# Optimization experiments

Hardware: AMD Instinct MI355X
Metric: run time of the kernel (lower is better)

Reference implementation:

```python
import jax, jax.numpy as jnp
import numpy as np

H = 1024
IN = 512
B = 32
E_H = 0.5
Z_MIN = 0.001
Z_MAX = 0.1
DT = 1.0


def setup_inputs() -> dict:
    key = jax.random.key(0)
    ks = jax.random.split(key, 10)
    s = 1.0 / np.sqrt(H)
    uni = lambda k, shape: jax.random.uniform(k, shape, jnp.float32, -s, s)
    return {
        "x": jax.random.normal(ks[0], (IN, B), jnp.float32),
        "h": jax.random.uniform(ks[1], (B, H), jnp.float32),      # hidden state [B,H]
        "X": jnp.ones((B, H, H), jnp.float32),                     # resources
        "U": jnp.full((B, H, H), 0.9, jnp.float32),                # utilization (init 0.9)
        "c_x": uni(ks[2], (H, H)),
        "c_u": uni(ks[3], (H, H)),
        "c_U": uni(ks[4], (H, H)),
        "c_h": uni(ks[5], (H, 1)),
        "w": uni(ks[6], (H, H)),
        "p": uni(ks[7], (H, IN)),
        "b": uni(ks[8], (H, 1)),
    }


def reference(x, h, X, U, c_x, c_u, c_U, c_h, w, p, b):
    sig = jax.nn.sigmoid
    hb = h[:, :, None]                                  # h[b,j] broadcast over k -> [B,H,1]
    # resource (X) update: z_x + (1-z_x)*X - dt*U*X*h
    z_x = Z_MIN + (Z_MAX - Z_MIN) * sig(c_x)            # [H,H]
    X_new = z_x + (1.0 - z_x) * X - DT * U * (X * hb)   # [B,H,H]
    # utilization (U) update, clamped to [Ucap (detached), 1]
    z_u = Z_MIN + (Z_MAX - Z_MIN) * sig(c_u)            # [H,H]
    Ucap = 0.9 * sig(c_U)                               # [H,H]
    U_new = Ucap * z_u + (1.0 - z_u) * U + DT * Ucap * ((1.0 - U) * hb)
    U_new = jnp.clip(U_new, jax.lax.stop_gradient(Ucap), 1.0)
    # hidden update with dynamic weights W = w * U * X (per batch)
    z_h = E_H * sig(c_h)                                # [H,1]
    W = w * U_new * X_new                               # [B,H,H]
    rec = jnp.einsum("bjk,bk->jb", W, h)               # [H,B]
    pre = rec + p @ x + b                               # [H,B]
    h_newT = (1.0 - z_h) * h.T + z_h * sig(pre)         # [H,B]
    return h_newT.T                                     # [B,H]
```

## Files before the change

### kernel.cpp

```cpp
#include <hip/hip_runtime.h>

#define HH 1024
#define INW 512
#define BB 32
#define BG 16
#define Z_MIN_C 0.001f
#define Z_RANGE_C 0.099f
#define E_H_C 0.5f

__device__ __forceinline__ float sigmoidf_(float v) {
    return 1.0f / (1.0f + __expf(-v));
}

__global__ __launch_bounds__(256) void stp_fused(
    const float* __restrict__ x,
    const float* __restrict__ h,
    const float* __restrict__ X,
    const float* __restrict__ U,
    const float* __restrict__ c_x,
    const float* __restrict__ c_u,
    const float* __restrict__ c_U,
    const float* __restrict__ c_h,
    const float* __restrict__ w,
    const float* __restrict__ p,
    const float* __restrict__ bias,
    float* __restrict__ out)
{
    const int j = blockIdx.x >> 1;
    const int g = blockIdx.x & 1;
    const int t = threadIdx.x;
    const int lane = t & 63;
    const int wave = t >> 6;

    __shared__ float px_part[16][BG];
    __shared__ float rec_part[BG][4];

    {
        const int b_id = t & 15;
        const int seg = t >> 4;
        float acc = 0.0f;
        const float* prow = p + j * INW + seg * 32;
        const float* xcol = x + seg * 32 * BB + (g * BG + b_id);
        #pragma unroll
        for (int i = 0; i < 32; ++i)
            acc = fmaf(prow[i], xcol[i * BB], acc);
        px_part[seg][b_id] = acc;
    }

    const int k0 = t * 4;
    float4 cx4 = *(const float4*)(c_x + j * HH + k0);
    float4 cu4 = *(const float4*)(c_u + j * HH + k0);
    float4 cC4 = *(const float4*)(c_U + j * HH + k0);
    float4 wv4 = *(const float4*)(w + j * HH + k0);
    const float* cxv = &cx4.x;
    const float* cuv = &cu4.x;
    const float* cCv = &cC4.x;
    const float* wvv = &wv4.x;

    float zx[4], ozx[4], Acoef[4], ozu[4], Uc[4], wr[4];
    #pragma unroll
    for (int c = 0; c < 4; ++c) {
        float zxx = Z_MIN_C + Z_RANGE_C * sigmoidf_(cxv[c]);
        float zuu = Z_MIN_C + Z_RANGE_C * sigmoidf_(cuv[c]);
        float ucc = 0.9f * sigmoidf_(cCv[c]);
        zx[c] = zxx;
        ozx[c] = 1.0f - zxx;
        ozu[c] = 1.0f - zuu;
        Uc[c] = ucc;
        Acoef[c] = ucc * zuu;
        wr[c] = wvv[c];
    }

    float s[BG];
    #pragma unroll
    for (int i = 0; i < BG; ++i) s[i] = 0.0f;

    for (int bb = 0; bb < BG; bb += 4) {
        float4 Xl[4], Ul[4], hk[4];
        float hj[4];
        #pragma unroll
        for (int i = 0; i < 4; ++i) {
            const int b = g * BG + bb + i;
            const int rowbase = (b * HH + j) * HH;
            Xl[i] = *(const float4*)(X + rowbase + k0);
            Ul[i] = *(const float4*)(U + rowbase + k0);
            hk[i] = *(const float4*)(h + b * HH + k0);
            hj[i] = h[b * HH + j];
        }
        #pragma unroll
        for (int i = 0; i < 4; ++i) {
            const float hjv = hj[i];
            const float* Xv = &Xl[i].x;
            const float* Uv = &Ul[i].x;
            const float* hkv = &hk[i].x;
            float ss = 0.0f;
            #pragma unroll
            for (int c = 0; c < 4; ++c) {
                float Xn = fmaf(ozx[c], Xv[c], zx[c]);
                Xn = fmaf(-Uv[c], Xv[c] * hjv, Xn);
                float Un = fmaf(ozu[c], Uv[c], Acoef[c]);
                Un = fmaf(Uc[c] * hjv, 1.0f - Uv[c], Un);
                Un = fminf(fmaxf(Un, Uc[c]), 1.0f);
                ss = fmaf(wr[c] * hkv[c], Un * Xn, ss);
            }
            s[bb + i] += ss;
        }
    }

    #pragma unroll
    for (int i = 0; i < BG; ++i) {
        float v = s[i];
        #pragma unroll
        for (int off = 32; off > 0; off >>= 1)
            v += __shfl_xor(v, off);
        if (lane == 0) rec_part[i][wave] = v;
    }
    __syncthreads();

    if (t < BG) {
        const int b = g * BG + t;
        float rec = rec_part[t][0] + rec_part[t][1] + rec_part[t][2] + rec_part[t][3];
        float px = 0.0f;
        #pragma unroll
        for (int sgi = 0; sgi < 16; ++sgi) px += px_part[sgi][t];
        float pre = rec + px + bias[j];
        float zh = E_H_C * sigmoidf_(c_h[j]);
        float hv = h[b * HH + j];
        out[b * HH + j] = (1.0f - zh) * hv + zh * sigmoidf_(pre);
    }
}

extern "C" void kernel_launch(void* const* d_in, const int* in_sizes, int n_in,
                              void* d_out, int out_size, void* d_ws, size_t ws_size,
                              hipStream_t stream) {
    const float* x   = (const float*)d_in[0];
    const float* h   = (const float*)d_in[1];
    const float* X   = (const float*)d_in[2];
    const float* U   = (const float*)d_in[3];
    const float* c_x = (const float*)d_in[4];
    const float* c_u = (const float*)d_in[5];
    const float* c_U = (const float*)d_in[6];
    const float* c_h = (const float*)d_in[7];
    const float* w   = (const float*)d_in[8];
    const float* p   = (const float*)d_in[9];
    const float* b   = (const float*)d_in[10];
    float* out = (float*)d_out;

    stp_fused<<<HH * 2, 256, 0, stream>>>(x, h, X, U, c_x, c_u, c_U, c_h, w, p, b, out);
}
```

Before: 334.2 us.

## Split batch into 4 groups, software-pipeline X/U loads with nontemporal prefetch

Each block now handles 8 batches instead of 16, and the grid grows to 4096 blocks ordered so that consecutive blocks share a batch group. The X/U row loads go through a 3-deep rotating register prefetch using nontemporal loads, and launch bounds request 4 blocks per SM so more memory is in flight for this bandwidth-bound stream. In exchange, the per-row parameters and the p@x projection are recomputed twice as often, adding redundant sigmoid and L2 traffic.

```diff
diff --git a/kernel.cpp b/kernel.cpp
--- a/kernel.cpp
+++ b/kernel.cpp
@@ -3,16 +3,18 @@
 #define HH 1024
 #define INW 512
 #define BB 32
-#define BG 16
+#define BG 8
 #define Z_MIN_C 0.001f
 #define Z_RANGE_C 0.099f
 #define E_H_C 0.5f
+
+typedef float v4f __attribute__((ext_vector_type(4)));
 
 __device__ __forceinline__ float sigmoidf_(float v) {
     return 1.0f / (1.0f + __expf(-v));
 }
 
-__global__ __launch_bounds__(256) void stp_fused(
+__global__ __launch_bounds__(256, 4) void stp_fused(
     const float* __restrict__ x,
     const float* __restrict__ h,
     const float* __restrict__ X,
@@ -26,85 +28,88 @@
     const float* __restrict__ bias,
     float* __restrict__ out)
 {
-    const int j = blockIdx.x >> 1;
-    const int g = blockIdx.x & 1;
+    const int j = blockIdx.x & (HH - 1);
+    const int g = blockIdx.x >> 10;
     const int t = threadIdx.x;
     const int lane = t & 63;
     const int wave = t >> 6;
 
-    __shared__ float px_part[16][BG];
+    __shared__ float px_part[32][BG];
     __shared__ float rec_part[BG][4];
 
     {
-        const int b_id = t & 15;
-        const int seg = t >> 4;
+        const int b_id = t & 7;
+        const int seg = t >> 3;
+        const int b = g * BG + b_id;
         float acc = 0.0f;
-        const float* prow = p + j * INW + seg * 32;
-        const float* xcol = x + seg * 32 * BB + (g * BG + b_id);
+        const float* prow = p + j * INW + seg * 16;
+        const float* xcol = x + (seg * 16) * BB + b;
         #pragma unroll
-        for (int i = 0; i < 32; ++i)
+        for (int i = 0; i < 16; ++i)
             acc = fmaf(prow[i], xcol[i * BB], acc);
         px_part[seg][b_id] = acc;
     }
 
     const int k0 = t * 4;
-    float4 cx4 = *(const float4*)(c_x + j * HH + k0);
-    float4 cu4 = *(const float4*)(c_u + j * HH + k0);
-    float4 cC4 = *(const float4*)(c_U + j * HH + k0);
-    float4 wv4 = *(const float4*)(w + j * HH + k0);
-    const float* cxv = &cx4.x;
-    const float* cuv = &cu4.x;
-    const float* cCv = &cC4.x;
-    const float* wvv = &wv4.x;
+    v4f cx4 = *(const v4f*)(c_x + j * HH + k0);
+    v4f cu4 = *(const v4f*)(c_u + j * HH + k0);
+    v4f cC4 = *(const v4f*)(c_U + j * HH + k0);
+    v4f wv4 = *(const v4f*)(w + j * HH + k0);
 
-    float zx[4], ozx[4], Acoef[4], ozu[4], Uc[4], wr[4];
+    float zx[4], ozx[4], Acoef[4], ozu[4], Ucap[4], wr[4];
     #pragma unroll
     for (int c = 0; c < 4; ++c) {
-        float zxx = Z_MIN_C + Z_RANGE_C * sigmoidf_(cxv[c]);
-        float zuu = Z_MIN_C + Z_RANGE_C * sigmoidf_(cuv[c]);
-        float ucc = 0.9f * sigmoidf_(cCv[c]);
+        float zxx = Z_MIN_C + Z_RANGE_C * sigmoidf_(cx4[c]);
+        float zuu = Z_MIN_C + Z_RANGE_C * sigmoidf_(cu4[c]);
+        float ucc = 0.9f * sigmoidf_(cC4[c]);
         zx[c] = zxx;
         ozx[c] = 1.0f - zxx;
         ozu[c] = 1.0f - zuu;
-        Uc[c] = ucc;
+        Ucap[c] = ucc;
         Acoef[c] = ucc * zuu;
-        wr[c] = wvv[c];
+        wr[c] = wv4[c];
     }
 
     float s[BG];
+    v4f Xb[3], Ub[3], hb[3];
+    float hjb[3];
+
     #pragma unroll
-    for (int i = 0; i < BG; ++i) s[i] = 0.0f;
+    for (int i = 0; i < 3; ++i) {
+        const int b = g * BG + i;
+        const int rb = (b * HH + j) * HH + k0;
+        Xb[i] = __builtin_nontemporal_load((const v4f*)(X + rb));
+        Ub[i] = __builtin_nontemporal_load((const v4f*)(U + rb));
+        hb[i] = *(const v4f*)(h + b * HH + k0);
+        hjb[i] = h[b * HH + j];
+    }
 
-    for (int bb = 0; bb < BG; bb += 4) {
-        float4 Xl[4], Ul[4], hk[4];
-        float hj[4];
+    #pragma unroll
+    for (int i = 0; i < BG; ++i) {
+        const int sl = i % 3;
+        v4f Xc = Xb[sl];
+        v4f Uc = Ub[sl];
+        v4f hc = hb[sl];
+        float hjv = hjb[sl];
+        if (i + 3 < BG) {
+            const int b = g * BG + i + 3;
+            const int rb = (b * HH + j) * HH + k0;
+            Xb[sl] = __builtin_nontemporal_load((const v4f*)(X + rb));
+            Ub[sl] = __builtin_nontemporal_load((const v4f*)(U + rb));
+            hb[sl] = *(const v4f*)(h + b * HH + k0);
+            hjb[sl] = h[b * HH + j];
+        }
+        float ss = 0.0f;
         #pragma unroll
-        for (int i = 0; i < 4; ++i) {
-            const int b = g * BG + bb + i;
-            const int rowbase = (b * HH + j) * HH;
-            Xl[i] = *(const float4*)(X + rowbase + k0);
-            Ul[i] = *(const float4*)(U + rowbase + k0);
-            hk[i] = *(const float4*)(h + b * HH + k0);
-            hj[i] = h[b * HH + j];
+        for (int c = 0; c < 4; ++c) {
+            float Xn = fmaf(ozx[c], Xc[c], zx[c]);
+            Xn = fmaf(-Uc[c], Xc[c] * hjv, Xn);
+            float Un = fmaf(ozu[c], Uc[c], Acoef[c]);
+            Un = fmaf(Ucap[c] * hjv, 1.0f - Uc[c], Un);
+            Un = fminf(fmaxf(Un, Ucap[c]), 1.0f);
+            ss = fmaf(wr[c] * hc[c], Un * Xn, ss);
         }
-        #pragma unroll
-        for (int i = 0; i < 4; ++i) {
-            const float hjv = hj[i];
-            const float* Xv = &Xl[i].x;
-            const float* Uv = &Ul[i].x;
-            const float* hkv = &hk[i].x;
-            float ss = 0.0f;
-            #pragma unroll
-            for (int c = 0; c < 4; ++c) {
-                float Xn = fmaf(ozx[c], Xv[c], zx[c]);
-                Xn = fmaf(-Uv[c], Xv[c] * hjv, Xn);
-                float Un = fmaf(ozu[c], Uv[c], Acoef[c]);
-                Un = fmaf(Uc[c] * hjv, 1.0f - Uv[c], Un);
-                Un = fminf(fmaxf(Un, Uc[c]), 1.0f);
-                ss = fmaf(wr[c] * hkv[c], Un * Xn, ss);
-            }
-            s[bb + i] += ss;
-        }
+        s[i] = ss;
     }
 
     #pragma unroll
@@ -122,7 +127,7 @@
         float rec = rec_part[t][0] + rec_part[t][1] + rec_part[t][2] + rec_part[t][3];
         float px = 0.0f;
         #pragma unroll
-        for (int sgi = 0; sgi < 16; ++sgi) px += px_part[sgi][t];
+        for (int sgi = 0; sgi < 32; ++sgi) px += px_part[sgi][t];
         float pre = rec + px + bias[j];
         float zh = E_H_C * sigmoidf_(c_h[j]);
         float hv = h[b * HH + j];
@@ -146,5 +151,5 @@
     const float* b   = (const float*)d_in[10];
     float* out = (float*)d_out;
 
-    stp_fused<<<HH * 2, 256, 0, stream>>>(x, h, X, U, c_x, c_u, c_U, c_h, w, p, b, out);
+    stp_fused<<<HH * 4, 256, 0, stream>>>(x, h, X, U, c_x, c_u, c_U, c_h, w, p, b, out);
 }
```

Result: faster. 291.6 us (-12.7%).
